# Performance work log

Measured on AMD Instinct MI355X. Metric: run time of the kernel, lower is better.

Reference implementation:

```python
import jax, jax.numpy as jnp
import numpy as np

N_NODES = 100000
N_EDGES = 6400000
IN_CH = 128
NEG_SLOPE = 0.2


def setup_inputs() -> dict:
    key = jax.random.key(0)
    k1, k2, k3, k4, k5 = jax.random.split(key, 5)
    x = jax.random.normal(k1, (N_NODES, IN_CH), dtype=jnp.float32)
    edge_index = jax.random.randint(k2, (2, N_EDGES), 0, N_NODES, dtype=jnp.int64)
    # GATConv params (heads=1, out_channels=1): glorot-style scale
    W = jax.random.normal(k3, (IN_CH, 1), dtype=jnp.float32) / np.sqrt(IN_CH)
    att_src = jax.random.normal(k4, (1,), dtype=jnp.float32)
    att_dst = jax.random.normal(k5, (1,), dtype=jnp.float32)
    bias = jnp.zeros((1,), dtype=jnp.float32)
    return {"x": x, "edge_index": edge_index, "W": W,
            "att_src": att_src, "att_dst": att_dst, "bias": bias}


def reference(x, edge_index, W, att_src, att_dst, bias):
    N = x.shape[0]
    h = (x @ W)[:, 0]                      # [N] projected features (out_channels=1)
    # add self-loops (PyG default add_self_loops=True)
    loop = jnp.arange(N, dtype=edge_index.dtype)
    src = jnp.concatenate([edge_index[0], loop])   # [E+N]
    dst = jnp.concatenate([edge_index[1], loop])
    a_s = h * att_src[0]                   # per-node src attention term
    a_d = h * att_dst[0]                   # per-node dst attention term
    logits = jax.nn.leaky_relu(a_s[src] + a_d[dst], NEG_SLOPE)  # [E+N]
    # segment softmax over incoming edges of each destination node
    seg_max = jax.ops.segment_max(logits, dst, num_segments=N)
    e = jnp.exp(logits - seg_max[dst])
    denom = jax.ops.segment_sum(e, dst, num_segments=N)
    alpha = e / (denom[dst] + 1e-16)
    # scatter-aggregate weighted source features
    out = jax.ops.segment_sum(alpha * h[src], dst, num_segments=N)  # [N]
    return out[:, None] + bias             # [N, 1]
```

## Files before the change

kernel.cpp:

```cpp
#include <hip/hip_runtime.h>

#define IN_CH 128
#define NEG_SLOPE 0.2f
#define BINSZ 8000
#define NBINS 13
#define NW 8192
#define MAX_SG 39
#define MAX_BPB 40
#define F_NUM 2097152.0f
#define F_DEN 16777216.0f
#define INV_F_NUM 4.76837158203125e-7f
#define INV_F_DEN 5.9604644775390625e-8f

typedef int   vi4 __attribute__((ext_vector_type(4)));
typedef float vf4 __attribute__((ext_vector_type(4)));

__device__ __forceinline__ float lrelu(float v) { return v > 0.f ? v : NEG_SLOPE * v; }
__device__ __forceinline__ unsigned enc_max(float f) {
    unsigned u = __float_as_uint(f);
    return (u & 0x80000000u) ? ~u : (u | 0x80000000u);
}
__device__ __forceinline__ float dec_max(unsigned e) {
    return (e & 0x80000000u) ? __uint_as_float(e ^ 0x80000000u) : __uint_as_float(~e);
}
__device__ __forceinline__ unsigned bf16_rne(float f) {
    unsigned u = __float_as_uint(f);
    return (u + 0x7FFFu + ((u >> 16) & 1u)) >> 16;
}

__device__ __forceinline__ void do_proj(const float* __restrict__ x, const float* __restrict__ W,
                                        const float* __restrict__ att_dst,
                                        float* __restrict__ h, float* __restrict__ ad_h,
                                        int n, int wid, int nwaves) {
    int lane = threadIdx.x & 63;
    int half = lane >> 5;
    int hl   = lane & 31;

    vf4 w4 = reinterpret_cast<const vf4*>(W)[hl];
    const float ad = att_dst[0];

    int npair = n >> 1;
    for (int p0 = wid * 4; p0 < npair; p0 += nwaves * 4) {
        float s[4];
        #pragma unroll
        for (int k = 0; k < 4; ++k) {
            int p = p0 + k;
            s[k] = 0.f;
            if (p < npair) {
                int row = 2 * p + half;
                vf4 v = __builtin_nontemporal_load(
                    reinterpret_cast<const vf4*>(x + (size_t)row * IN_CH) + hl);
                s[k] = v.x * w4.x + v.y * w4.y + v.z * w4.z + v.w * w4.w;
            }
        }
        #pragma unroll
        for (int k = 0; k < 4; ++k) {
            #pragma unroll
            for (int off = 16; off > 0; off >>= 1) s[k] += __shfl_xor(s[k], off);
        }
        #pragma unroll
        for (int k = 0; k < 4; ++k) {
            int p = p0 + k;
            if (p < npair && hl == 0) {
                int row = 2 * p + half;
                h[row] = s[k];
                ad_h[row] = s[k] * ad;
            }
        }
    }
    if ((n & 1) && wid == 0) {
        int row = n - 1;
        vf4 v = reinterpret_cast<const vf4*>(x + (size_t)row * IN_CH)[hl];
        float s = v.x * w4.x + v.y * w4.y + v.z * w4.z + v.w * w4.w;
        #pragma unroll
        for (int off = 16; off > 0; off >>= 1) s += __shfl_xor(s, off);
        if (lane == 0) { h[row] = s; ad_h[row] = s * ad; }
    }
}

__global__ __launch_bounds__(256)
void proj_kernel(const float* __restrict__ x, const float* __restrict__ W,
                 const float* __restrict__ att_dst,
                 float* __restrict__ h, float* __restrict__ ad_h, int n) {
    int wid    = (blockIdx.x * blockDim.x + threadIdx.x) >> 6;
    int nwaves = (gridDim.x * blockDim.x) >> 6;
    do_proj(x, W, att_dst, h, ad_h, n, wid, nwaves);
}

__global__ __launch_bounds__(256)
void count_proj_kernel(const int* __restrict__ dst_idx, int* __restrict__ wc, int E,
                       const float* __restrict__ x, const float* __restrict__ W,
                       const float* __restrict__ att_dst,
                       float* __restrict__ h, float* __restrict__ ad_h, int n) {
    int b = blockIdx.x;
    int role = b % 3;
    if (role == 2) {
        int qid = b / 3;
        int wid = qid * 4 + (threadIdx.x >> 6);
        do_proj(x, W, att_dst, h, ad_h, n, wid, 4096);
        return;
    }
    int pid  = (b / 3) * 2 + role;
    int lane = threadIdx.x & 63, wv = threadIdx.x >> 6;
    int g = pid * 4 + wv;
    long long E4 = E >> 2;
    long long e0 = 4 * (E4 * g / NW);
    long long e1 = (g == NW - 1) ? (long long)E : 4 * (E4 * (g + 1) / NW);

    int cnt = 0;
    for (long long i0 = e0; i0 < e1; i0 += 64) {
        long long i = i0 + lane;
        int bb = NBINS;
        if (i < e1) bb = __builtin_nontemporal_load(dst_idx + i) / BINSZ;
        #pragma unroll
        for (int b2 = 0; b2 < NBINS; ++b2) {
            unsigned long long m = __ballot(bb == b2);
            if (lane == b2) cnt += __popcll(m);
        }
    }
    if (lane < NBINS) wc[lane * NW + g] = cnt;
}

__global__ __launch_bounds__(256)
void hmax_kernel(const float* __restrict__ h,
                 const float* __restrict__ att_src, const float* __restrict__ att_dst,
                 unsigned* __restrict__ maxenc, int n) {
    const float as = att_src[0];
    const float ad = att_dst[0];
    float m1 = -1e30f, m2 = -1e30f;
    for (int i = blockIdx.x * blockDim.x + threadIdx.x; i < n;
         i += gridDim.x * blockDim.x) {
        float v = h[i];
        m1 = fmaxf(m1, v * as);
        m2 = fmaxf(m2, v * ad);
    }
    #pragma unroll
    for (int off = 32; off > 0; off >>= 1) {
        m1 = fmaxf(m1, __shfl_xor(m1, off));
        m2 = fmaxf(m2, __shfl_xor(m2, off));
    }
    __shared__ float bm[2][4];
    int wv = threadIdx.x >> 6;
    if ((threadIdx.x & 63) == 0) { bm[0][wv] = m1; bm[1][wv] = m2; }
    __syncthreads();
    if (threadIdx.x == 0) {
        float a = fmaxf(fmaxf(bm[0][0], bm[0][1]), fmaxf(bm[0][2], bm[0][3]));
        float b = fmaxf(fmaxf(bm[1][0], bm[1][1]), fmaxf(bm[1][2], bm[1][3]));
        atomicMax(maxenc,     enc_max(a));
        atomicMax(maxenc + 1, enc_max(b));
    }
}

__global__ __launch_bounds__(256)
void scanA_kernel(const int* __restrict__ wc, int* __restrict__ bsum) {
    __shared__ int wt[4];
    int t = threadIdx.x, lane = t & 63, wv = t >> 6;
    vi4 c = *reinterpret_cast<const vi4*>(wc + blockIdx.x * 1024 + 4 * t);
    int s = c.x + c.y + c.z + c.w;
    #pragma unroll
    for (int off = 32; off > 0; off >>= 1) s += __shfl_xor(s, off);
    if (lane == 0) wt[wv] = s;
    __syncthreads();
    if (t == 0) bsum[blockIdx.x] = wt[0] + wt[1] + wt[2] + wt[3];
}

__global__ __launch_bounds__(128)
void scanB_kernel(const int* __restrict__ bsum, int* __restrict__ bbase,
                  int* __restrict__ rbase, int* __restrict__ hist, int nchunk) {
    __shared__ int sb[129];
    __shared__ int wt[2];
    int t = threadIdx.x, lane = t & 63, wv = t >> 6;
    int v = (t < nchunk) ? bsum[t] : 0;
    int inc = v;
    #pragma unroll
    for (int d2 = 1; d2 < 64; d2 <<= 1) { int u = __shfl_up(inc, d2); if (lane >= d2) inc += u; }
    if (lane == 63) wt[wv] = inc;
    __syncthreads();
    int excl = ((wv == 1) ? wt[0] : 0) + inc - v;
    sb[t] = excl;
    if (t == 127) sb[128] = excl + v;
    __syncthreads();
    if (t < nchunk) bbase[t] = sb[t];
    if (t < NBINS) {
        int rb = sb[t * (NW / 1024)];
        rbase[t] = rb;
        int nb = (t == NBINS - 1) ? sb[128] : sb[(t + 1) * (NW / 1024)];
        hist[t] = nb - rb;
    }
}

__global__ __launch_bounds__(256)
void scanC_kernel(const int* __restrict__ wc, const int* __restrict__ bbase,
                  int* __restrict__ wbase) {
    __shared__ int wt[4];
    int t = threadIdx.x, lane = t & 63, wv = t >> 6;
    int base = blockIdx.x * 1024 + 4 * t;
    vi4 c = *reinterpret_cast<const vi4*>(wc + base);
    int s0 = c.x, s1 = s0 + c.y, s2 = s1 + c.z, s3 = s2 + c.w;
    int tot = s3;
    int inc = tot;
    #pragma unroll
    for (int d2 = 1; d2 < 64; d2 <<= 1) { int u = __shfl_up(inc, d2); if (lane >= d2) inc += u; }
    if (lane == 63) wt[wv] = inc;
    __syncthreads();
    int wb = 0;
    for (int k = 0; k < wv; ++k) wb += wt[k];
    int excl = bbase[blockIdx.x] + wb + inc - tot;
    vi4 o; o.x = excl; o.y = excl + s0; o.z = excl + s1; o.w = excl + s2;
    *reinterpret_cast<vi4*>(wbase + base) = o;
}

__global__ __launch_bounds__(256)
void place_kernel(const int* __restrict__ src_idx, const int* __restrict__ dst_idx,
                  const float* __restrict__ h,
                  const int* __restrict__ wbase, unsigned* __restrict__ rec, int E) {
    __shared__ int ccur[4][NBINS];
    int lane = threadIdx.x & 63, wv = threadIdx.x >> 6;
    int g = blockIdx.x * 4 + wv;
    if (lane < NBINS) ccur[wv][lane] = wbase[lane * NW + g];
    __syncthreads();

    long long E4 = E >> 2;
    long long e0 = 4 * (E4 * g / NW);
    long long e1 = (g == NW - 1) ? (long long)E : 4 * (E4 * (g + 1) / NW);
    for (long long i0 = e0; i0 < e1; i0 += 256) {
        long long i = i0 + 4 * lane;
        if (i < e1) {
            vi4 d4 = __builtin_nontemporal_load(reinterpret_cast<const vi4*>(dst_idx + i));
            vi4 s4 = __builtin_nontemporal_load(reinterpret_cast<const vi4*>(src_idx + i));
            float h0 = h[s4.x], h1 = h[s4.y], h2 = h[s4.z], h3 = h[s4.w];
            int b0 = d4.x / BINSZ, b1 = d4.y / BINSZ, b2 = d4.z / BINSZ, b3 = d4.w / BINSZ;
            int p0 = atomicAdd(&ccur[wv][b0], 1);
            int p1 = atomicAdd(&ccur[wv][b1], 1);
            int p2 = atomicAdd(&ccur[wv][b2], 1);
            int p3 = atomicAdd(&ccur[wv][b3], 1);
            rec[p0] = ((unsigned)(d4.x - b0 * BINSZ) << 16) | bf16_rne(h0);
            rec[p1] = ((unsigned)(d4.y - b1 * BINSZ) << 16) | bf16_rne(h1);
            rec[p2] = ((unsigned)(d4.z - b2 * BINSZ) << 16) | bf16_rne(h2);
            rec[p3] = ((unsigned)(d4.w - b3 * BINSZ) << 16) | bf16_rne(h3);
        }
    }
}

__global__ __launch_bounds__(1024)
void gather_kernel(const unsigned* __restrict__ rec,
                   const float* __restrict__ ad_h,
                   const float* __restrict__ att_src, const unsigned* __restrict__ maxenc,
                   const int* __restrict__ rbase, const int* __restrict__ hist,
                   unsigned long long* __restrict__ part, int SG) {
    __shared__ __align__(16) unsigned long long s_acc[BINSZ];

    int bin   = blockIdx.x / SG;
    int slice = blockIdx.x - bin * SG;
    long long r0 = rbase[bin];
    int cnt   = hist[bin];
    long long g0 = r0 + (long long)cnt * slice / SG;
    long long g1 = r0 + (long long)cnt * (slice + 1) / SG;

    {
        vi4 z = {0, 0, 0, 0};
        for (int k = threadIdx.x; k < BINSZ / 2; k += 1024)
            *reinterpret_cast<vi4*>(&s_acc[2 * k]) = z;
    }
    __syncthreads();

    const float as = att_src[0];
    const float L  = lrelu(dec_max(maxenc[0]) + dec_max(maxenc[1]));
    const float* adw = ad_h + bin * BINSZ;

    auto process1 = [&](unsigned q) {
        int ri = q >> 16;
        float h0 = __uint_as_float(q << 16);
        float e0 = __expf(lrelu(fmaf(h0, as, adw[ri])) - L);
        unsigned long long p0 = ((unsigned long long)(long long)__float2int_rn(e0 * h0 * F_NUM) << 32)
                              + __float2uint_rn(e0 * F_DEN);
        atomicAdd(&s_acc[ri], p0);
    };

    long long a0 = (g0 + 3) & ~3LL;
    long long a1 = g1 & ~3LL;
    long long headEnd, tail0;
    if (a0 <= a1) { headEnd = a0; tail0 = a1; }
    else          { headEnd = g1; tail0 = g1; a0 = 0; a1 = 0; }

    for (long long i = g0 + threadIdx.x; i < headEnd; i += 1024) process1(rec[i]);

    long long i = a0 + 4 * (long long)threadIdx.x;
    vi4 q = {0,0,0,0};
    bool have = (i < a1);
    if (have) q = __builtin_nontemporal_load(reinterpret_cast<const vi4*>(rec + i));
    while (have) {
        long long nx = i + 4096;
        bool nhave = (nx < a1);
        vi4 nq = {0,0,0,0};
        if (nhave) nq = __builtin_nontemporal_load(reinterpret_cast<const vi4*>(rec + nx));
        unsigned u0=(unsigned)q.x, u1=(unsigned)q.y, u2=(unsigned)q.z, u3=(unsigned)q.w;
        int r0i=u0>>16, r1i=u1>>16, r2i=u2>>16, r3i=u3>>16;
        float h0=__uint_as_float(u0<<16), h1=__uint_as_float(u1<<16);
        float h2=__uint_as_float(u2<<16), h3=__uint_as_float(u3<<16);
        float e0 = __expf(lrelu(fmaf(h0, as, adw[r0i])) - L);
        float e1 = __expf(lrelu(fmaf(h1, as, adw[r1i])) - L);
        float e2 = __expf(lrelu(fmaf(h2, as, adw[r2i])) - L);
        float e3 = __expf(lrelu(fmaf(h3, as, adw[r3i])) - L);
        unsigned long long p0 = ((unsigned long long)(long long)__float2int_rn(e0 * h0 * F_NUM) << 32) + __float2uint_rn(e0 * F_DEN);
        unsigned long long p1 = ((unsigned long long)(long long)__float2int_rn(e1 * h1 * F_NUM) << 32) + __float2uint_rn(e1 * F_DEN);
        unsigned long long p2 = ((unsigned long long)(long long)__float2int_rn(e2 * h2 * F_NUM) << 32) + __float2uint_rn(e2 * F_DEN);
        unsigned long long p3 = ((unsigned long long)(long long)__float2int_rn(e3 * h3 * F_NUM) << 32) + __float2uint_rn(e3 * F_DEN);
        atomicAdd(&s_acc[r0i], p0);
        atomicAdd(&s_acc[r1i], p1);
        atomicAdd(&s_acc[r2i], p2);
        atomicAdd(&s_acc[r3i], p3);
        i = nx; q = nq; have = nhave;
    }

    for (long long i2 = tail0 + threadIdx.x; i2 < g1; i2 += 1024) process1(rec[i2]);
    __syncthreads();

    unsigned long long* outp = part + (size_t)blockIdx.x * BINSZ;
    for (int k = threadIdx.x; k < BINSZ / 2; k += 1024) {
        vi4 v = *reinterpret_cast<const vi4*>(&s_acc[2 * k]);
        __builtin_nontemporal_store(v, reinterpret_cast<vi4*>(outp + 2 * k));
    }
}

__global__ void reduce_final(const unsigned long long* __restrict__ part,
                             const float* __restrict__ h,
                             const float* __restrict__ att_src, const float* __restrict__ att_dst,
                             const float* __restrict__ bias, const unsigned* __restrict__ maxenc,
                             float* __restrict__ out, int n, int SG) {
    int i = blockIdx.x * blockDim.x + threadIdx.x;
    if (i >= n) return;
    int bin = i / BINSZ;
    int off = i - bin * BINSZ;
    float num = 0.f, den = 0.f;
    const unsigned long long* p = part + (size_t)(bin * SG) * BINSZ;
    for (int s = 0; s < SG; ++s) {
        unsigned long long v = __builtin_nontemporal_load(p + off);
        num += (float)(int)(v >> 32);
        den += (float)(unsigned)(v & 0xffffffffULL);
        p += BINSZ;
    }
    num *= INV_F_NUM;
    den *= INV_F_DEN;
    const float L = lrelu(dec_max(maxenc[0]) + dec_max(maxenc[1]));
    float hv = h[i];
    float e  = __expf(lrelu(hv * (att_src[0] + att_dst[0])) - L);
    out[i] = (num + e * hv) / (den + e + 1e-30f) + bias[0];
}

__global__ __launch_bounds__(1024)
void binpass_kernel(const int* __restrict__ src_idx, const int* __restrict__ dst_idx,
                    const float* __restrict__ h,
                    const float* __restrict__ att_src, const float* __restrict__ att_dst,
                    float* __restrict__ part, int E, int n, int BPB) {
    __shared__ float s_num[BINSZ];
    __shared__ float s_den[BINSZ];

    int bin   = blockIdx.x / BPB;
    int slice = blockIdx.x - bin * BPB;
    int base  = bin * BINSZ;
    int blen  = min(BINSZ, n - base);

    for (int k = threadIdx.x; k < BINSZ; k += 1024) { s_num[k] = 0.f; s_den[k] = 0.f; }
    __syncthreads();

    const float as = att_src[0];
    const float ad = att_dst[0];

    long long e0 = (long long)E * slice / BPB;
    long long e1 = (long long)E * (slice + 1) / BPB;
    for (long long i = e0 + threadIdx.x; i < e1; i += 1024) {
        int d = dst_idx[i];
        unsigned r = (unsigned)(d - base);
        if (r < (unsigned)blen) {
            int s = src_idx[i];
            float hs = h[s];
            float v  = fmaf(hs, as, h[d] * ad);
            float e  = __expf(lrelu(v));
            atomicAdd(&s_num[r], e * hs);
            atomicAdd(&s_den[r], e);
        }
    }
    __syncthreads();

    float* outp = part + (size_t)blockIdx.x * (2 * BINSZ);
    for (int k = threadIdx.x; k < BINSZ; k += 1024) {
        outp[k]         = s_num[k];
        outp[BINSZ + k] = s_den[k];
    }
}

__global__ void fb_reduce_final(const float* __restrict__ part, const float* __restrict__ h,
                                const float* __restrict__ att_src, const float* __restrict__ att_dst,
                                const float* __restrict__ bias, float* __restrict__ out,
                                int n, int BPB) {
    int i = blockIdx.x * blockDim.x + threadIdx.x;
    if (i >= n) return;
    int bin = i / BINSZ;
    int off = i - bin * BINSZ;
    float num = 0.f, den = 0.f;
    const float* p = part + (size_t)(bin * BPB) * (2 * BINSZ);
    for (int s = 0; s < BPB; ++s) {
        num += p[off];
        den += p[BINSZ + off];
        p += 2 * BINSZ;
    }
    float hv = h[i];
    float e  = __expf(lrelu(hv * (att_src[0] + att_dst[0])));
    out[i] = (num + e * hv) / (den + e + 1e-16f) + bias[0];
}

__global__ void edge_kernel(const int* __restrict__ src_idx, const int* __restrict__ dst_idx,
                            const float* __restrict__ h,
                            const float* __restrict__ att_src, const float* __restrict__ att_dst,
                            float* __restrict__ nd, int E) {
    const float as = att_src[0];
    const float ad = att_dst[0];
    int i      = blockIdx.x * blockDim.x + threadIdx.x;
    int stride = gridDim.x * blockDim.x;
    for (; i < E; i += stride) {
        int s = src_idx[i];
        int d = dst_idx[i];
        float hs = h[s];
        float e  = __expf(lrelu(fmaf(hs, as, h[d] * ad)));
        unsafeAtomicAdd(&nd[2 * d],     e * hs);
        unsafeAtomicAdd(&nd[2 * d + 1], e);
    }
}

__global__ void final_kernel(const float* __restrict__ h, const float* __restrict__ nd,
                             const float* __restrict__ att_src, const float* __restrict__ att_dst,
                             const float* __restrict__ bias, float* __restrict__ out, int n) {
    int i = blockIdx.x * blockDim.x + threadIdx.x;
    if (i >= n) return;
    float hv = h[i];
    float e  = __expf(lrelu(hv * (att_src[0] + att_dst[0])));
    out[i] = (nd[2 * i] + e * hv) / (nd[2 * i + 1] + e + 1e-16f) + bias[0];
}

extern "C" void kernel_launch(void* const* d_in, const int* in_sizes, int n_in,
                              void* d_out, int out_size, void* d_ws, size_t ws_size,
                              hipStream_t stream) {
    const float* x       = (const float*)d_in[0];
    const int*   ei      = (const int*)d_in[1];
    const float* W       = (const float*)d_in[2];
    const float* att_src = (const float*)d_in[3];
    const float* att_dst = (const float*)d_in[4];
    const float* bias    = (const float*)d_in[5];
    float*       out     = (float*)d_out;

    const int n = out_size;
    const int E = in_sizes[1] / 2;

    const int NELEM  = NBINS * NW;
    const int NCHUNK = NELEM / 1024;

    size_t off = 0;
    auto alloc = [&](size_t bytes) { size_t p = off; off = (off + bytes + 255) & ~(size_t)255; return p; };
    size_t o_h    = alloc((size_t)n * sizeof(float));
    size_t o_adh  = alloc((size_t)n * sizeof(float));
    size_t o_wc   = alloc((size_t)NELEM * sizeof(int));
    size_t o_wb   = alloc((size_t)NELEM * sizeof(int));
    size_t o_bs   = alloc((size_t)NCHUNK * sizeof(int));
    size_t o_bb   = alloc((size_t)NCHUNK * sizeof(int));
    size_t o_meta = alloc(64 * sizeof(int));
    size_t o_rec  = alloc((size_t)E * sizeof(unsigned));
    size_t fixed  = off;

    float*    h      = (float*)((char*)d_ws + o_h);
    float*    ad_h   = (float*)((char*)d_ws + o_adh);
    int*      rbase  = (int*)((char*)d_ws + o_meta);
    int*      hist   = rbase + 16;
    unsigned* maxenc = (unsigned*)(rbase + 32);
    const size_t per = (size_t)BINSZ * sizeof(unsigned long long);

    int SG = 0;
    if (ws_size > fixed) SG = (int)((ws_size - fixed) / ((size_t)NBINS * per));
    if (SG > MAX_SG) SG = MAX_SG;

    bool ok_shape = (n <= NBINS * BINSZ) && ((E & 3) == 0) && (E >= 4 * NW) && ((n & 1) == 0);

    if (SG >= 8 && ok_shape) {
        int*                wc   = (int*)((char*)d_ws + o_wc);
        int*                wb   = (int*)((char*)d_ws + o_wb);
        int*                bsum = (int*)((char*)d_ws + o_bs);
        int*                bbase= (int*)((char*)d_ws + o_bb);
        unsigned*           rec  = (unsigned*)((char*)d_ws + o_rec);
        unsigned long long* part = (unsigned long long*)((char*)d_ws + fixed);

        hipMemsetAsync(maxenc, 0, 2 * sizeof(unsigned), stream);
        count_proj_kernel<<<3072, 256, 0, stream>>>(ei + E, wc, E,
                                                    x, W, att_dst, h, ad_h, n);
        scanA_kernel<<<NCHUNK, 256, 0, stream>>>(wc, bsum);
        scanB_kernel<<<1, 128, 0, stream>>>(bsum, bbase, rbase, hist, NCHUNK);
        scanC_kernel<<<NCHUNK, 256, 0, stream>>>(wc, bbase, wb);
        place_kernel<<<NW / 4, 256, 0, stream>>>(ei, ei + E, h, wb, rec, E);
        hmax_kernel<<<120, 256, 0, stream>>>(h, att_src, att_dst, maxenc, n);
        gather_kernel<<<NBINS * SG, 1024, 0, stream>>>(rec, ad_h, att_src, maxenc,
                                                       rbase, hist, part, SG);
        reduce_final<<<(n + 255) / 256, 256, 0, stream>>>(part, h, att_src, att_dst,
                                                          bias, maxenc, out, n, SG);
    } else {
        proj_kernel<<<1024, 256, 0, stream>>>(x, W, att_dst, h, ad_h, n);
        size_t hb = (((size_t)n * 2 * sizeof(float)) + 255) & ~(size_t)255;
        int BPB = 0;
        if (ws_size > hb) BPB = (int)((ws_size - hb) / ((size_t)NBINS * per));
        if (BPB > MAX_BPB) BPB = MAX_BPB;

        if (BPB >= 6 && n <= NBINS * BINSZ) {
            float* part = (float*)((char*)d_ws + hb);
            binpass_kernel<<<NBINS * BPB, 1024, 0, stream>>>(
                ei, ei + E, h, att_src, att_dst, part, E, n, BPB);
            fb_reduce_final<<<(n + 255) / 256, 256, 0, stream>>>(
                part, h, att_src, att_dst, bias, out, n, BPB);
        } else {
            float* nd = (float*)((char*)d_ws + hb);
            hipMemsetAsync(nd, 0, (size_t)n * 2 * sizeof(float), stream);
            edge_kernel<<<2048, 256, 0, stream>>>(ei, ei + E, h, att_src, att_dst, nd, E);
            final_kernel<<<(n + 255) / 256, 256, 0, stream>>>(h, nd, att_src, att_dst,
                                                              bias, out, n);
        }
    }
}
```

Before: 134.1 us.

## Fuse hmax into place kernel, fold max reset into scan, prefetch place loads

Merges the per-node max reduction into the place kernel as extra blocks, so it runs alongside edge placement instead of as its own launch. The memset of the max accumulators moves into the single-block scanB kernel, which removes another API call. The place loop is also software-pipelined: the next iteration's index vectors are loaded before the current batch is processed, to hide load latency. Together these cut launch overhead and add overlap, at the cost of more register pressure in the place kernel.

```diff
diff --git a/kernel.cpp b/kernel.cpp
--- a/kernel.cpp
+++ b/kernel.cpp
@@ -7,6 +7,8 @@
 #define NW 8192
 #define MAX_SG 39
 #define MAX_BPB 40
+#define PLACE_BLOCKS (NW / 4)
+#define HMAX_BLOCKS 120
 #define F_NUM 2097152.0f
 #define F_DEN 16777216.0f
 #define INV_F_NUM 4.76837158203125e-7f
@@ -122,36 +124,6 @@
 }
 
 __global__ __launch_bounds__(256)
-void hmax_kernel(const float* __restrict__ h,
-                 const float* __restrict__ att_src, const float* __restrict__ att_dst,
-                 unsigned* __restrict__ maxenc, int n) {
-    const float as = att_src[0];
-    const float ad = att_dst[0];
-    float m1 = -1e30f, m2 = -1e30f;
-    for (int i = blockIdx.x * blockDim.x + threadIdx.x; i < n;
-         i += gridDim.x * blockDim.x) {
-        float v = h[i];
-        m1 = fmaxf(m1, v * as);
-        m2 = fmaxf(m2, v * ad);
-    }
-    #pragma unroll
-    for (int off = 32; off > 0; off >>= 1) {
-        m1 = fmaxf(m1, __shfl_xor(m1, off));
-        m2 = fmaxf(m2, __shfl_xor(m2, off));
-    }
-    __shared__ float bm[2][4];
-    int wv = threadIdx.x >> 6;
-    if ((threadIdx.x & 63) == 0) { bm[0][wv] = m1; bm[1][wv] = m2; }
-    __syncthreads();
-    if (threadIdx.x == 0) {
-        float a = fmaxf(fmaxf(bm[0][0], bm[0][1]), fmaxf(bm[0][2], bm[0][3]));
-        float b = fmaxf(fmaxf(bm[1][0], bm[1][1]), fmaxf(bm[1][2], bm[1][3]));
-        atomicMax(maxenc,     enc_max(a));
-        atomicMax(maxenc + 1, enc_max(b));
-    }
-}
-
-__global__ __launch_bounds__(256)
 void scanA_kernel(const int* __restrict__ wc, int* __restrict__ bsum) {
     __shared__ int wt[4];
     int t = threadIdx.x, lane = t & 63, wv = t >> 6;
@@ -166,10 +138,12 @@
 
 __global__ __launch_bounds__(128)
 void scanB_kernel(const int* __restrict__ bsum, int* __restrict__ bbase,
-                  int* __restrict__ rbase, int* __restrict__ hist, int nchunk) {
+                  int* __restrict__ rbase, int* __restrict__ hist,
+                  unsigned* __restrict__ maxenc, int nchunk) {
     __shared__ int sb[129];
     __shared__ int wt[2];
     int t = threadIdx.x, lane = t & 63, wv = t >> 6;
+    if (t < 2) maxenc[t] = 0u;
     int v = (t < nchunk) ? bsum[t] : 0;
     int inc = v;
     #pragma unroll
@@ -211,34 +185,76 @@
 }
 
 __global__ __launch_bounds__(256)
-void place_kernel(const int* __restrict__ src_idx, const int* __restrict__ dst_idx,
-                  const float* __restrict__ h,
-                  const int* __restrict__ wbase, unsigned* __restrict__ rec, int E) {
+void place_hmax_kernel(const int* __restrict__ src_idx, const int* __restrict__ dst_idx,
+                       const float* __restrict__ h, const int* __restrict__ wbase,
+                       unsigned* __restrict__ rec, int E,
+                       const float* __restrict__ att_src, const float* __restrict__ att_dst,
+                       unsigned* __restrict__ maxenc, int n) {
+    int b = blockIdx.x;
+    if (b >= PLACE_BLOCKS) {
+        int bid = b - PLACE_BLOCKS;
+        const float as = att_src[0];
+        const float ad = att_dst[0];
+        float m1 = -1e30f, m2 = -1e30f;
+        for (int i = bid * 256 + threadIdx.x; i < n; i += HMAX_BLOCKS * 256) {
+            float v = h[i];
+            m1 = fmaxf(m1, v * as);
+            m2 = fmaxf(m2, v * ad);
+        }
+        #pragma unroll
+        for (int off = 32; off > 0; off >>= 1) {
+            m1 = fmaxf(m1, __shfl_xor(m1, off));
+            m2 = fmaxf(m2, __shfl_xor(m2, off));
+        }
+        __shared__ float bm[2][4];
+        int wv = threadIdx.x >> 6;
+        if ((threadIdx.x & 63) == 0) { bm[0][wv] = m1; bm[1][wv] = m2; }
+        __syncthreads();
+        if (threadIdx.x == 0) {
+            float a = fmaxf(fmaxf(bm[0][0], bm[0][1]), fmaxf(bm[0][2], bm[0][3]));
+            float bmax = fmaxf(fmaxf(bm[1][0], bm[1][1]), fmaxf(bm[1][2], bm[1][3]));
+            atomicMax(maxenc,     enc_max(a));
+            atomicMax(maxenc + 1, enc_max(bmax));
+        }
+        return;
+    }
+
     __shared__ int ccur[4][NBINS];
     int lane = threadIdx.x & 63, wv = threadIdx.x >> 6;
-    int g = blockIdx.x * 4 + wv;
+    int g = b * 4 + wv;
     if (lane < NBINS) ccur[wv][lane] = wbase[lane * NW + g];
     __syncthreads();
 
     long long E4 = E >> 2;
     long long e0 = 4 * (E4 * g / NW);
     long long e1 = (g == NW - 1) ? (long long)E : 4 * (E4 * (g + 1) / NW);
-    for (long long i0 = e0; i0 < e1; i0 += 256) {
-        long long i = i0 + 4 * lane;
-        if (i < e1) {
-            vi4 d4 = __builtin_nontemporal_load(reinterpret_cast<const vi4*>(dst_idx + i));
-            vi4 s4 = __builtin_nontemporal_load(reinterpret_cast<const vi4*>(src_idx + i));
-            float h0 = h[s4.x], h1 = h[s4.y], h2 = h[s4.z], h3 = h[s4.w];
-            int b0 = d4.x / BINSZ, b1 = d4.y / BINSZ, b2 = d4.z / BINSZ, b3 = d4.w / BINSZ;
-            int p0 = atomicAdd(&ccur[wv][b0], 1);
-            int p1 = atomicAdd(&ccur[wv][b1], 1);
-            int p2 = atomicAdd(&ccur[wv][b2], 1);
-            int p3 = atomicAdd(&ccur[wv][b3], 1);
-            rec[p0] = ((unsigned)(d4.x - b0 * BINSZ) << 16) | bf16_rne(h0);
-            rec[p1] = ((unsigned)(d4.y - b1 * BINSZ) << 16) | bf16_rne(h1);
-            rec[p2] = ((unsigned)(d4.z - b2 * BINSZ) << 16) | bf16_rne(h2);
-            rec[p3] = ((unsigned)(d4.w - b3 * BINSZ) << 16) | bf16_rne(h3);
-        }
+
+    long long i = e0 + 4 * (long long)lane;
+    bool have = (i < e1);
+    vi4 d4 = {0,0,0,0}, s4 = {0,0,0,0};
+    if (have) {
+        d4 = __builtin_nontemporal_load(reinterpret_cast<const vi4*>(dst_idx + i));
+        s4 = __builtin_nontemporal_load(reinterpret_cast<const vi4*>(src_idx + i));
+    }
+    while (have) {
+        long long nx = i + 256;
+        bool nhave = (nx < e1);
+        vi4 d4n = {0,0,0,0}, s4n = {0,0,0,0};
+        if (nhave) {
+            d4n = __builtin_nontemporal_load(reinterpret_cast<const vi4*>(dst_idx + nx));
+            s4n = __builtin_nontemporal_load(reinterpret_cast<const vi4*>(src_idx + nx));
+        }
+        float h0 = h[s4.x], h1 = h[s4.y], h2 = h[s4.z], h3 = h[s4.w];
+        int b0 = d4.x / BINSZ, b1 = d4.y / BINSZ, b2 = d4.z / BINSZ, b3 = d4.w / BINSZ;
+        int p0 = atomicAdd(&ccur[wv][b0], 1);
+        int p1 = atomicAdd(&ccur[wv][b1], 1);
+        int p2 = atomicAdd(&ccur[wv][b2], 1);
+        int p3 = atomicAdd(&ccur[wv][b3], 1);
+        rec[p0] = ((unsigned)(d4.x - b0 * BINSZ) << 16) | bf16_rne(h0);
+        rec[p1] = ((unsigned)(d4.y - b1 * BINSZ) << 16) | bf16_rne(h1);
+        rec[p2] = ((unsigned)(d4.z - b2 * BINSZ) << 16) | bf16_rne(h2);
+        rec[p3] = ((unsigned)(d4.w - b3 * BINSZ) << 16) | bf16_rne(h3);
+        i = nx; d4 = d4n; s4 = s4n; have = nhave;
     }
 }
 
@@ -488,14 +504,13 @@
         unsigned*           rec  = (unsigned*)((char*)d_ws + o_rec);
         unsigned long long* part = (unsigned long long*)((char*)d_ws + fixed);
 
-        hipMemsetAsync(maxenc, 0, 2 * sizeof(unsigned), stream);
         count_proj_kernel<<<3072, 256, 0, stream>>>(ei + E, wc, E,
                                                     x, W, att_dst, h, ad_h, n);
         scanA_kernel<<<NCHUNK, 256, 0, stream>>>(wc, bsum);
-        scanB_kernel<<<1, 128, 0, stream>>>(bsum, bbase, rbase, hist, NCHUNK);
+        scanB_kernel<<<1, 128, 0, stream>>>(bsum, bbase, rbase, hist, maxenc, NCHUNK);
         scanC_kernel<<<NCHUNK, 256, 0, stream>>>(wc, bbase, wb);
-        place_kernel<<<NW / 4, 256, 0, stream>>>(ei, ei + E, h, wb, rec, E);
-        hmax_kernel<<<120, 256, 0, stream>>>(h, att_src, att_dst, maxenc, n);
+        place_hmax_kernel<<<PLACE_BLOCKS + HMAX_BLOCKS, 256, 0, stream>>>(
+            ei, ei + E, h, wb, rec, E, att_src, att_dst, maxenc, n);
         gather_kernel<<<NBINS * SG, 1024, 0, stream>>>(rec, ad_h, att_src, maxenc,
                                                        rbase, hist, part, SG);
         reduce_final<<<(n + 255) / 256, 256, 0, stream>>>(part, h, att_src, att_dst,
```

Result: faster. 121.6 us (-9.4%).
